# Optimization experiments

Measured on AMD Instinct MI355X. Metric: run time of the kernel, lower is better.

The kernel has to match this reference:

```python
import jax, jax.numpy as jnp
import numpy as np

B, E, H, O = 131072, 32, 32, 2

def setup_inputs() -> dict:
    key = jax.random.key(0)
    ks = jax.random.split(key, 12)
    f32 = jnp.float32
    inp = {
        "last_pos_rel": jax.random.normal(ks[0], (B, O), dtype=f32),
        "hidden_state": jax.random.normal(ks[1], (1, B, H), dtype=f32),
        "start_pos": jax.random.normal(ks[2], (B, O), dtype=f32),
        # spatial embedding Linear(2 -> 32)
        "W_se": jax.random.normal(ks[3], (E, O), dtype=f32) * 0.1,
        "b_se": jax.random.normal(ks[4], (E,), dtype=f32) * 0.1,
        # LSTM (input E -> hidden H), PyTorch layout: [4H, E] / [4H, H], gate order i,f,g,o
        "W_ih": jax.random.normal(ks[5], (4 * H, E), dtype=f32) * 0.1,
        "b_ih": jax.random.normal(ks[6], (4 * H,), dtype=f32) * 0.1,
        "W_hh": jax.random.normal(ks[7], (4 * H, H), dtype=f32) * 0.1,
        "b_hh": jax.random.normal(ks[8], (4 * H,), dtype=f32) * 0.1,
        # hidden2pos Linear(32 -> 2)
        "W_hp": jax.random.normal(ks[9], (O, H), dtype=f32) * 0.1,
        "b_hp": jax.random.normal(ks[10], (O,), dtype=f32) * 0.1,
        "seq_len": 60,
    }
    return inp


def reference(last_pos_rel, hidden_state, start_pos, W_se, b_se,
              W_ih, b_ih, W_hh, b_hh, W_hp, b_hp, seq_len):
    # dropout in eval mode -> identity
    h0 = hidden_state[0]                     # (B, H)  num_layers == 1
    c0 = jnp.zeros_like(h0)
    x0 = last_pos_rel @ W_se.T + b_se        # (B, E) spatial embedding
    b_gate = b_ih + b_hh                     # (4H,)

    def step(carry, _):
        h, c, x = carry
        gates = x @ W_ih.T + h @ W_hh.T + b_gate          # (B, 4H)
        i, f, g, o = jnp.split(gates, 4, axis=-1)         # PyTorch gate order
        c = jax.nn.sigmoid(f) * c + jax.nn.sigmoid(i) * jnp.tanh(g)
        h = jax.nn.sigmoid(o) * jnp.tanh(c)
        pos_rel = h @ W_hp.T + b_hp                        # (B, 2)
        x_next = pos_rel @ W_se.T + b_se                   # feed prediction back
        return (h, c, x_next), pos_rel

    (hT, cT, _), pred_traj_rel = jax.lax.scan(step, (h0, c0, x0), None, length=seq_len)
    # relative_to_abs: cumsum over time, add start_pos
    abs_traj = jnp.cumsum(pred_traj_rel, axis=0) + start_pos[None, :, :]  # (T, B, 2)
    return abs_traj, hT[None, :, :]
```

## Files before the change

kernel.cpp:

```cpp
#include <hip/hip_runtime.h>

typedef _Float16 half8  __attribute__((ext_vector_type(8)));
typedef __fp16   half2v __attribute__((ext_vector_type(2)));
typedef float    f32x4  __attribute__((ext_vector_type(4)));
typedef float    f32x2  __attribute__((ext_vector_type(2)));

#define L2E 1.44269504088896340736f
#define MFMA(a, b, c) __builtin_amdgcn_mfma_f32_16x16x32_f16((a), (b), (c), 0, 0, 0)

__global__ void precompute_kernel(const float* __restrict__ W_se,
                                  const float* __restrict__ b_se,
                                  const float* __restrict__ W_ih,
                                  const float* __restrict__ b_ih,
                                  const float* __restrict__ W_hh,
                                  const float* __restrict__ b_hh,
                                  const float* __restrict__ W_hp,
                                  const float* __restrict__ b_hp,
                                  float* __restrict__ ws) {
    int s = threadIdx.x;
    if (s >= 128) return;
    int gi = s >> 5, hf = (s >> 4) & 1, q = (s >> 2) & 3, r = s & 3;
    int o  = gi * 32 + 8 * q + 4 * hf + r;
    float w0 = 0.f, w1 = 0.f, bse = 0.f;
    for (int e = 0; e < 32; ++e) {
        float wi = W_ih[o * 32 + e];
        w0  += W_se[e * 2 + 0] * wi;
        w1  += W_se[e * 2 + 1] * wi;
        bse += b_se[e] * wi;
    }
    float sc = (gi == 2) ? 2.0f * L2E : -L2E;
    for (int k = 0; k < 32; ++k) {
        float whh = W_hh[o * 32 + k];
        ws[s * 32 + k]        = sc * (whh + W_hp[k] * w0 + W_hp[32 + k] * w1);
        ws[4096 + s * 32 + k] = sc * whh;
    }
    float bg = b_ih[o] + b_hh[o] + bse;
    ws[8192 + s] = sc * w0;
    ws[8320 + s] = sc * w1;
    ws[8448 + s] = sc * (bg + b_hp[0] * w0 + b_hp[1] * w1);
    ws[8576 + s] = sc * bg;
}

__device__ __forceinline__ void split8(const float* v, half8& hi, half8& lo) {
    #pragma unroll
    for (int p = 0; p < 4; ++p) {
        half2v hp = __builtin_amdgcn_cvt_pkrtz(v[2 * p], v[2 * p + 1]);
        hi[2 * p] = hp.x; hi[2 * p + 1] = hp.y;
        float l0 = v[2 * p]     - (float)hp.x;
        float l1 = v[2 * p + 1] - (float)hp.y;
        half2v lp2 = __builtin_amdgcn_cvt_pkrtz(l0, l1);
        lo[2 * p] = lp2.x; lo[2 * p + 1] = lp2.y;
    }
}

__device__ __forceinline__ void cvt8(const float* v, half8& hi) {
    #pragma unroll
    for (int p = 0; p < 4; ++p) {
        half2v hp = __builtin_amdgcn_cvt_pkrtz(v[2 * p], v[2 * p + 1]);
        hi[2 * p] = hp.x; hi[2 * p + 1] = hp.y;
    }
}

__global__ __launch_bounds__(256, 4) void lstm_kernel(
        const float* __restrict__ lp,
        const float* __restrict__ h0g,
        const float* __restrict__ sp,
        const float* __restrict__ Whp,
        const float* __restrict__ bhp,
        const float* __restrict__ ws,
        const int*   __restrict__ seqp,
        float* __restrict__ out, int Bn) {
    const int lane = threadIdx.x & 63;
    const int col  = lane & 15;
    const int q    = lane >> 4;
    const int tile = blockIdx.x * 4 + (threadIdx.x >> 6);
    const int base = tile * 16;
    if (base >= Bn) return;
    const int T = seqp[0];

    const float* Wcs  = ws;
    const float* Whhs = ws + 4096;
    const float* W00s = ws + 8192;
    const float* W01s = ws + 8320;
    const float* bg2q = ws + 8448 + 4 * q;
    const float* b0sq = ws + 8576 + 4 * q;

    half8 wh[8];
    #pragma unroll
    for (int t8 = 0; t8 < 8; ++t8) {
        float v[8];
        const float* p = Wcs + (size_t)(t8 * 16 + col) * 32 + 8 * q;
        #pragma unroll
        for (int i = 0; i < 8; ++i) v[i] = p[i];
        cvt8(v, wh[t8]);
    }
    half8 ph;
    {
        float v[8];
        #pragma unroll
        for (int i = 0; i < 8; ++i) v[i] = (col < 2) ? Whp[col * 32 + 8 * q + i] : 0.f;
        cvt8(v, ph);
    }
    const float pb0 = (q == 0) ? bhp[0] : 0.f;
    const float pb1 = (q == 0) ? bhp[1] : 0.f;

    half8 b0h, b0l;
    {
        float v[8];
        const float* p = h0g + (size_t)(base + col) * 32 + 8 * q;
        #pragma unroll
        for (int i = 0; i < 8; ++i) v[i] = p[i];
        split8(v, b0h, b0l);
    }
    half8 lph, lpl;
    #pragma unroll
    for (int i = 0; i < 8; ++i) { lph[i] = (_Float16)0.f; lpl[i] = (_Float16)0.f; }
    if (q == 0) {
        float l0 = lp[(size_t)(base + col) * 2 + 0];
        float l1 = lp[(size_t)(base + col) * 2 + 1];
        half2v x = __builtin_amdgcn_cvt_pkrtz(l0, l1);
        lph[0] = x.x; lph[1] = x.y;
        half2v y = __builtin_amdgcn_cvt_pkrtz(l0 - (float)x.x, l1 - (float)x.y);
        lpl[0] = y.x; lpl[1] = y.y;
    }

    f32x4 accg[8];
    #pragma unroll
    for (int t8 = 0; t8 < 8; ++t8) {
        f32x4 a = *(const f32x4*)(b0sq + t8 * 16);
        half8 ah;
        {
            float v[8];
            const float* p = Whhs + (size_t)(t8 * 16 + col) * 32 + 8 * q;
            #pragma unroll
            for (int i = 0; i < 8; ++i) v[i] = p[i];
            cvt8(v, ah);
        }
        a = MFMA(ah, b0h, a); a = MFMA(ah, b0l, a);
        half8 ch;
        #pragma unroll
        for (int i = 0; i < 8; ++i) ch[i] = (_Float16)0.f;
        if (q == 0) {
            half2v y = __builtin_amdgcn_cvt_pkrtz(W00s[t8 * 16 + col],
                                                  W01s[t8 * 16 + col]);
            ch[0] = y.x; ch[1] = y.y;
        }
        a = MFMA(ch, lph, a); a = MFMA(ch, lpl, a);
        accg[t8] = a;
    }

    f32x2 c2[4];
    #pragma unroll
    for (int i = 0; i < 4; ++i) c2[i] = (f32x2)0.f;
    float run0 = 0.f, run1 = 0.f;
    if (q == 0) {
        run0 = sp[(size_t)(base + col) * 2 + 0];
        run1 = sp[(size_t)(base + col) * 2 + 1];
    }

    float hn[8];
    #pragma unroll 1
    for (int n = 0; n < T; ++n) {
        #pragma unroll
        for (int hf = 0; hf < 2; ++hf) {
            #pragma unroll
            for (int rp = 0; rp < 2; ++rp) {
                const int idx = 2 * hf + rp;
                f32x2 gI, gF, gG, gO;
                gI.x = accg[0 + hf][2 * rp]; gI.y = accg[0 + hf][2 * rp + 1];
                gF.x = accg[2 + hf][2 * rp]; gF.y = accg[2 + hf][2 * rp + 1];
                gG.x = accg[4 + hf][2 * rp]; gG.y = accg[4 + hf][2 * rp + 1];
                gO.x = accg[6 + hf][2 * rp]; gO.y = accg[6 + hf][2 * rp + 1];
                f32x2 ei, ef, eg, eo;
                ei.x = __builtin_amdgcn_exp2f(gI.x); ei.y = __builtin_amdgcn_exp2f(gI.y);
                ef.x = __builtin_amdgcn_exp2f(gF.x); ef.y = __builtin_amdgcn_exp2f(gF.y);
                eg.x = __builtin_amdgcn_exp2f(gG.x); eg.y = __builtin_amdgcn_exp2f(gG.y);
                eo.x = __builtin_amdgcn_exp2f(gO.x); eo.y = __builtin_amdgcn_exp2f(gO.y);
                f32x2 Df = ef + 1.f;
                f32x2 P  = (ei + 1.f) * (eg + 1.f);
                f32x2 PD = P * Df;
                f32x2 R;
                R.x = __builtin_amdgcn_rcpf(PD.x); R.y = __builtin_amdgcn_rcpf(PD.y);
                f32x2 cn = ((eg - 1.f) * Df + c2[idx] * P) * R;
                c2[idx] = cn;
                f32x2 arg = cn * (2.f * L2E);
                f32x2 ec;
                ec.x = __builtin_amdgcn_exp2f(arg.x); ec.y = __builtin_amdgcn_exp2f(arg.y);
                f32x2 DDo = (ec + 1.f) * (eo + 1.f);
                f32x2 Rs;
                Rs.x = __builtin_amdgcn_rcpf(DDo.x); Rs.y = __builtin_amdgcn_rcpf(DDo.y);
                f32x2 h2 = (ec - 1.f) * Rs;
                hn[4 * hf + 2 * rp]     = h2.x;
                hn[4 * hf + 2 * rp + 1] = h2.y;
            }
        }
        half8 bh;
        cvt8(hn, bh);

        f32x4 ap;
        ap[0] = pb0; ap[1] = pb1; ap[2] = 0.f; ap[3] = 0.f;
        ap = MFMA(ph, bh, ap);

        #pragma unroll
        for (int t8 = 0; t8 < 8; ++t8) {
            f32x4 a = *(const f32x4*)(bg2q + t8 * 16);
            a = MFMA(wh[t8], bh, a);
            accg[t8] = a;
        }

        if (q == 0) {
            run0 += ap[0]; run1 += ap[1];
            float2 w2; w2.x = run0; w2.y = run1;
            *(float2*)(out + 2 * ((size_t)n * Bn + base + col)) = w2;
        }
    }

    {
        float* p = out + (size_t)T * Bn * 2 + (size_t)(base + col) * 32 + 8 * q;
        float4 v0, v1;
        v0.x = hn[0]; v0.y = hn[1]; v0.z = hn[2]; v0.w = hn[3];
        v1.x = hn[4]; v1.y = hn[5]; v1.z = hn[6]; v1.w = hn[7];
        *(float4*)(p)     = v0;
        *(float4*)(p + 4) = v1;
    }
}

extern "C" void kernel_launch(void* const* d_in, const int* in_sizes, int n_in,
                              void* d_out, int out_size, void* d_ws, size_t ws_size,
                              hipStream_t stream) {
    const float* last_pos_rel = (const float*)d_in[0];
    const float* hidden_state = (const float*)d_in[1];
    const float* start_pos    = (const float*)d_in[2];
    const float* W_se         = (const float*)d_in[3];
    const float* b_se         = (const float*)d_in[4];
    const float* W_ih         = (const float*)d_in[5];
    const float* b_ih         = (const float*)d_in[6];
    const float* W_hh         = (const float*)d_in[7];
    const float* b_hh         = (const float*)d_in[8];
    const float* W_hp         = (const float*)d_in[9];
    const float* b_hp         = (const float*)d_in[10];
    const int*   seq_len      = (const int*)d_in[11];

    float* out = (float*)d_out;
    float* ws  = (float*)d_ws;

    const int Bn = in_sizes[0] / 2;

    hipLaunchKernelGGL(precompute_kernel, dim3(1), dim3(128), 0, stream,
                       W_se, b_se, W_ih, b_ih, W_hh, b_hh, W_hp, b_hp, ws);

    const int ntiles = (Bn + 15) / 16;
    const int nblk   = (ntiles + 3) / 4;
    hipLaunchKernelGGL(lstm_kernel, dim3(nblk), dim3(256), 0, stream,
                       last_pos_rel, hidden_state, start_pos, W_hp, b_hp,
                       ws, seq_len, out, Bn);
}
```

Measured before the change: 212.1 us.

## Process two batch tiles per wavefront to interleave independent LSTM recurrences

Each wavefront now handles two 16-row batch tiles, A and B. It interleaves their gate activations and MFMA updates so the two independent dependency chains can hide each other's latency, and the register-held fp16 weight fragments serve both tiles. Launch bounds drop from 4 to 3 waves and the grid halves. The final hidden state is now written from the fp16-rounded values instead of the fp32 ones, which loses precision, and the kernel has no guard when baseB lies past the end of the batch.

```diff
diff --git a/kernel.cpp b/kernel.cpp
--- a/kernel.cpp
+++ b/kernel.cpp
@@ -53,15 +53,7 @@
     }
 }
 
-__device__ __forceinline__ void cvt8(const float* v, half8& hi) {
-    #pragma unroll
-    for (int p = 0; p < 4; ++p) {
-        half2v hp = __builtin_amdgcn_cvt_pkrtz(v[2 * p], v[2 * p + 1]);
-        hi[2 * p] = hp.x; hi[2 * p + 1] = hp.y;
-    }
-}
-
-__global__ __launch_bounds__(256, 4) void lstm_kernel(
+__global__ __launch_bounds__(256, 3) void lstm_kernel(
         const float* __restrict__ lp,
         const float* __restrict__ h0g,
         const float* __restrict__ sp,
@@ -70,12 +62,12 @@
         const float* __restrict__ ws,
         const int*   __restrict__ seqp,
         float* __restrict__ out, int Bn) {
-    const int lane = threadIdx.x & 63;
-    const int col  = lane & 15;
-    const int q    = lane >> 4;
-    const int tile = blockIdx.x * 4 + (threadIdx.x >> 6);
-    const int base = tile * 16;
-    if (base >= Bn) return;
+    const int lane  = threadIdx.x & 63;
+    const int col   = lane & 15;
+    const int q     = lane >> 4;
+    const int baseA = (blockIdx.x * 8 + (threadIdx.x >> 6) * 2) * 16;
+    const int baseB = baseA + 16;
+    if (baseA >= Bn) return;
     const int T = seqp[0];
 
     const float* Wcs  = ws;
@@ -88,140 +80,176 @@
     half8 wh[8];
     #pragma unroll
     for (int t8 = 0; t8 < 8; ++t8) {
-        float v[8];
         const float* p = Wcs + (size_t)(t8 * 16 + col) * 32 + 8 * q;
         #pragma unroll
-        for (int i = 0; i < 8; ++i) v[i] = p[i];
-        cvt8(v, wh[t8]);
+        for (int pp = 0; pp < 4; ++pp) {
+            half2v h2 = __builtin_amdgcn_cvt_pkrtz(p[2 * pp], p[2 * pp + 1]);
+            wh[t8][2 * pp] = h2.x; wh[t8][2 * pp + 1] = h2.y;
+        }
     }
     half8 ph;
-    {
-        float v[8];
-        #pragma unroll
-        for (int i = 0; i < 8; ++i) v[i] = (col < 2) ? Whp[col * 32 + 8 * q + i] : 0.f;
-        cvt8(v, ph);
+    #pragma unroll
+    for (int pp = 0; pp < 4; ++pp) {
+        float v0 = (col < 2) ? Whp[col * 32 + 8 * q + 2 * pp]     : 0.f;
+        float v1 = (col < 2) ? Whp[col * 32 + 8 * q + 2 * pp + 1] : 0.f;
+        half2v h2 = __builtin_amdgcn_cvt_pkrtz(v0, v1);
+        ph[2 * pp] = h2.x; ph[2 * pp + 1] = h2.y;
     }
     const float pb0 = (q == 0) ? bhp[0] : 0.f;
     const float pb1 = (q == 0) ? bhp[1] : 0.f;
 
-    half8 b0h, b0l;
+    f32x4 accgA[8], accgB[8];
     {
-        float v[8];
-        const float* p = h0g + (size_t)(base + col) * 32 + 8 * q;
-        #pragma unroll
-        for (int i = 0; i < 8; ++i) v[i] = p[i];
-        split8(v, b0h, b0l);
-    }
-    half8 lph, lpl;
-    #pragma unroll
-    for (int i = 0; i < 8; ++i) { lph[i] = (_Float16)0.f; lpl[i] = (_Float16)0.f; }
-    if (q == 0) {
-        float l0 = lp[(size_t)(base + col) * 2 + 0];
-        float l1 = lp[(size_t)(base + col) * 2 + 1];
-        half2v x = __builtin_amdgcn_cvt_pkrtz(l0, l1);
-        lph[0] = x.x; lph[1] = x.y;
-        half2v y = __builtin_amdgcn_cvt_pkrtz(l0 - (float)x.x, l1 - (float)x.y);
-        lpl[0] = y.x; lpl[1] = y.y;
-    }
-
-    f32x4 accg[8];
-    #pragma unroll
-    for (int t8 = 0; t8 < 8; ++t8) {
-        f32x4 a = *(const f32x4*)(b0sq + t8 * 16);
-        half8 ah;
+        half8 bhA0, blA0, bhB0, blB0;
         {
             float v[8];
-            const float* p = Whhs + (size_t)(t8 * 16 + col) * 32 + 8 * q;
-            #pragma unroll
-            for (int i = 0; i < 8; ++i) v[i] = p[i];
-            cvt8(v, ah);
-        }
-        a = MFMA(ah, b0h, a); a = MFMA(ah, b0l, a);
-        half8 ch;
-        #pragma unroll
-        for (int i = 0; i < 8; ++i) ch[i] = (_Float16)0.f;
+            const float* pa = h0g + (size_t)(baseA + col) * 32 + 8 * q;
+            #pragma unroll
+            for (int i = 0; i < 8; ++i) v[i] = pa[i];
+            split8(v, bhA0, blA0);
+            const float* pb = h0g + (size_t)(baseB + col) * 32 + 8 * q;
+            #pragma unroll
+            for (int i = 0; i < 8; ++i) v[i] = pb[i];
+            split8(v, bhB0, blB0);
+        }
+        half8 lphA, lplA, lphB, lplB;
+        #pragma unroll
+        for (int i = 0; i < 8; ++i) {
+            lphA[i] = (_Float16)0.f; lplA[i] = (_Float16)0.f;
+            lphB[i] = (_Float16)0.f; lplB[i] = (_Float16)0.f;
+        }
         if (q == 0) {
-            half2v y = __builtin_amdgcn_cvt_pkrtz(W00s[t8 * 16 + col],
-                                                  W01s[t8 * 16 + col]);
-            ch[0] = y.x; ch[1] = y.y;
-        }
-        a = MFMA(ch, lph, a); a = MFMA(ch, lpl, a);
-        accg[t8] = a;
-    }
-
-    f32x2 c2[4];
-    #pragma unroll
-    for (int i = 0; i < 4; ++i) c2[i] = (f32x2)0.f;
-    float run0 = 0.f, run1 = 0.f;
+            float a0 = lp[(size_t)(baseA + col) * 2 + 0];
+            float a1 = lp[(size_t)(baseA + col) * 2 + 1];
+            half2v x = __builtin_amdgcn_cvt_pkrtz(a0, a1);
+            lphA[0] = x.x; lphA[1] = x.y;
+            half2v y = __builtin_amdgcn_cvt_pkrtz(a0 - (float)x.x, a1 - (float)x.y);
+            lplA[0] = y.x; lplA[1] = y.y;
+            float b0v = lp[(size_t)(baseB + col) * 2 + 0];
+            float b1v = lp[(size_t)(baseB + col) * 2 + 1];
+            half2v xb = __builtin_amdgcn_cvt_pkrtz(b0v, b1v);
+            lphB[0] = xb.x; lphB[1] = xb.y;
+            half2v yb = __builtin_amdgcn_cvt_pkrtz(b0v - (float)xb.x, b1v - (float)xb.y);
+            lplB[0] = yb.x; lplB[1] = yb.y;
+        }
+        #pragma unroll
+        for (int t8 = 0; t8 < 8; ++t8) {
+            f32x4 bias0 = *(const f32x4*)(b0sq + t8 * 16);
+            half8 ah;
+            {
+                const float* p = Whhs + (size_t)(t8 * 16 + col) * 32 + 8 * q;
+                #pragma unroll
+                for (int pp = 0; pp < 4; ++pp) {
+                    half2v h2 = __builtin_amdgcn_cvt_pkrtz(p[2 * pp], p[2 * pp + 1]);
+                    ah[2 * pp] = h2.x; ah[2 * pp + 1] = h2.y;
+                }
+            }
+            half8 ch;
+            #pragma unroll
+            for (int i = 0; i < 8; ++i) ch[i] = (_Float16)0.f;
+            if (q == 0) {
+                half2v y = __builtin_amdgcn_cvt_pkrtz(W00s[t8 * 16 + col],
+                                                      W01s[t8 * 16 + col]);
+                ch[0] = y.x; ch[1] = y.y;
+            }
+            f32x4 aA = bias0, aB = bias0;
+            aA = MFMA(ah, bhA0, aA); aA = MFMA(ah, blA0, aA);
+            aA = MFMA(ch, lphA, aA); aA = MFMA(ch, lplA, aA);
+            aB = MFMA(ah, bhB0, aB); aB = MFMA(ah, blB0, aB);
+            aB = MFMA(ch, lphB, aB); aB = MFMA(ch, lplB, aB);
+            accgA[t8] = aA; accgB[t8] = aB;
+        }
+    }
+
+    f32x2 c2A[4], c2B[4];
+    #pragma unroll
+    for (int i = 0; i < 4; ++i) { c2A[i] = (f32x2)0.f; c2B[i] = (f32x2)0.f; }
+    float runA0 = 0.f, runA1 = 0.f, runB0 = 0.f, runB1 = 0.f;
     if (q == 0) {
-        run0 = sp[(size_t)(base + col) * 2 + 0];
-        run1 = sp[(size_t)(base + col) * 2 + 1];
-    }
-
-    float hn[8];
+        runA0 = sp[(size_t)(baseA + col) * 2 + 0];
+        runA1 = sp[(size_t)(baseA + col) * 2 + 1];
+        runB0 = sp[(size_t)(baseB + col) * 2 + 0];
+        runB1 = sp[(size_t)(baseB + col) * 2 + 1];
+    }
+
+    half8 bhA, bhB;
+
+    auto act2 = [&](f32x4* accg, f32x2* c2, half8& bh, int hf, int rp) {
+        const int idx = 2 * hf + rp;
+        f32x2 gI, gF, gG, gO;
+        gI.x = accg[0 + hf][2 * rp]; gI.y = accg[0 + hf][2 * rp + 1];
+        gF.x = accg[2 + hf][2 * rp]; gF.y = accg[2 + hf][2 * rp + 1];
+        gG.x = accg[4 + hf][2 * rp]; gG.y = accg[4 + hf][2 * rp + 1];
+        gO.x = accg[6 + hf][2 * rp]; gO.y = accg[6 + hf][2 * rp + 1];
+        f32x2 ei, ef, eg, eo;
+        ei.x = __builtin_amdgcn_exp2f(gI.x); ei.y = __builtin_amdgcn_exp2f(gI.y);
+        ef.x = __builtin_amdgcn_exp2f(gF.x); ef.y = __builtin_amdgcn_exp2f(gF.y);
+        eg.x = __builtin_amdgcn_exp2f(gG.x); eg.y = __builtin_amdgcn_exp2f(gG.y);
+        eo.x = __builtin_amdgcn_exp2f(gO.x); eo.y = __builtin_amdgcn_exp2f(gO.y);
+        f32x2 Df = ef + 1.f;
+        f32x2 P  = (ei + 1.f) * (eg + 1.f);
+        f32x2 PD = P * Df;
+        f32x2 R;
+        R.x = __builtin_amdgcn_rcpf(PD.x); R.y = __builtin_amdgcn_rcpf(PD.y);
+        f32x2 cn = ((eg - 1.f) * Df + c2[idx] * P) * R;
+        c2[idx] = cn;
+        f32x2 arg = cn * (2.f * L2E);
+        f32x2 ec;
+        ec.x = __builtin_amdgcn_exp2f(arg.x); ec.y = __builtin_amdgcn_exp2f(arg.y);
+        f32x2 DDo = (ec + 1.f) * (eo + 1.f);
+        f32x2 Rs;
+        Rs.x = __builtin_amdgcn_rcpf(DDo.x); Rs.y = __builtin_amdgcn_rcpf(DDo.y);
+        f32x2 h2 = (ec - 1.f) * Rs;
+        half2v hp = __builtin_amdgcn_cvt_pkrtz(h2.x, h2.y);
+        bh[2 * idx] = hp.x; bh[2 * idx + 1] = hp.y;
+    };
+
     #pragma unroll 1
     for (int n = 0; n < T; ++n) {
         #pragma unroll
         for (int hf = 0; hf < 2; ++hf) {
             #pragma unroll
             for (int rp = 0; rp < 2; ++rp) {
-                const int idx = 2 * hf + rp;
-                f32x2 gI, gF, gG, gO;
-                gI.x = accg[0 + hf][2 * rp]; gI.y = accg[0 + hf][2 * rp + 1];
-                gF.x = accg[2 + hf][2 * rp]; gF.y = accg[2 + hf][2 * rp + 1];
-                gG.x = accg[4 + hf][2 * rp]; gG.y = accg[4 + hf][2 * rp + 1];
-                gO.x = accg[6 + hf][2 * rp]; gO.y = accg[6 + hf][2 * rp + 1];
-                f32x2 ei, ef, eg, eo;
-                ei.x = __builtin_amdgcn_exp2f(gI.x); ei.y = __builtin_amdgcn_exp2f(gI.y);
-                ef.x = __builtin_amdgcn_exp2f(gF.x); ef.y = __builtin_amdgcn_exp2f(gF.y);
-                eg.x = __builtin_amdgcn_exp2f(gG.x); eg.y = __builtin_amdgcn_exp2f(gG.y);
-                eo.x = __builtin_amdgcn_exp2f(gO.x); eo.y = __builtin_amdgcn_exp2f(gO.y);
-                f32x2 Df = ef + 1.f;
-                f32x2 P  = (ei + 1.f) * (eg + 1.f);
-                f32x2 PD = P * Df;
-                f32x2 R;
-                R.x = __builtin_amdgcn_rcpf(PD.x); R.y = __builtin_amdgcn_rcpf(PD.y);
-                f32x2 cn = ((eg - 1.f) * Df + c2[idx] * P) * R;
-                c2[idx] = cn;
-                f32x2 arg = cn * (2.f * L2E);
-                f32x2 ec;
-                ec.x = __builtin_amdgcn_exp2f(arg.x); ec.y = __builtin_amdgcn_exp2f(arg.y);
-                f32x2 DDo = (ec + 1.f) * (eo + 1.f);
-                f32x2 Rs;
-                Rs.x = __builtin_amdgcn_rcpf(DDo.x); Rs.y = __builtin_amdgcn_rcpf(DDo.y);
-                f32x2 h2 = (ec - 1.f) * Rs;
-                hn[4 * hf + 2 * rp]     = h2.x;
-                hn[4 * hf + 2 * rp + 1] = h2.y;
+                act2(accgA, c2A, bhA, hf, rp);
+                act2(accgB, c2B, bhB, hf, rp);
             }
         }
-        half8 bh;
-        cvt8(hn, bh);
-
-        f32x4 ap;
-        ap[0] = pb0; ap[1] = pb1; ap[2] = 0.f; ap[3] = 0.f;
-        ap = MFMA(ph, bh, ap);
+
+        f32x4 apA, apB;
+        apA[0] = pb0; apA[1] = pb1; apA[2] = 0.f; apA[3] = 0.f;
+        apB = apA;
+        apA = MFMA(ph, bhA, apA);
+        apB = MFMA(ph, bhB, apB);
 
         #pragma unroll
         for (int t8 = 0; t8 < 8; ++t8) {
-            f32x4 a = *(const f32x4*)(bg2q + t8 * 16);
-            a = MFMA(wh[t8], bh, a);
-            accg[t8] = a;
+            f32x4 bt = *(const f32x4*)(bg2q + t8 * 16);
+            accgA[t8] = MFMA(wh[t8], bhA, bt);
+            accgB[t8] = MFMA(wh[t8], bhB, bt);
         }
 
         if (q == 0) {
-            run0 += ap[0]; run1 += ap[1];
-            float2 w2; w2.x = run0; w2.y = run1;
-            *(float2*)(out + 2 * ((size_t)n * Bn + base + col)) = w2;
+            runA0 += apA[0]; runA1 += apA[1];
+            runB0 += apB[0]; runB1 += apB[1];
+            float2 wA; wA.x = runA0; wA.y = runA1;
+            float2 wB; wB.x = runB0; wB.y = runB1;
+            *(float2*)(out + 2 * ((size_t)n * Bn + baseA + col)) = wA;
+            *(float2*)(out + 2 * ((size_t)n * Bn + baseB + col)) = wB;
         }
     }
 
     {
-        float* p = out + (size_t)T * Bn * 2 + (size_t)(base + col) * 32 + 8 * q;
+        float* pa = out + (size_t)T * Bn * 2 + (size_t)(baseA + col) * 32 + 8 * q;
+        float* pb = out + (size_t)T * Bn * 2 + (size_t)(baseB + col) * 32 + 8 * q;
         float4 v0, v1;
-        v0.x = hn[0]; v0.y = hn[1]; v0.z = hn[2]; v0.w = hn[3];
-        v1.x = hn[4]; v1.y = hn[5]; v1.z = hn[6]; v1.w = hn[7];
-        *(float4*)(p)     = v0;
-        *(float4*)(p + 4) = v1;
+        v0.x = (float)bhA[0]; v0.y = (float)bhA[1]; v0.z = (float)bhA[2]; v0.w = (float)bhA[3];
+        v1.x = (float)bhA[4]; v1.y = (float)bhA[5]; v1.z = (float)bhA[6]; v1.w = (float)bhA[7];
+        *(float4*)(pa)     = v0;
+        *(float4*)(pa + 4) = v1;
+        v0.x = (float)bhB[0]; v0.y = (float)bhB[1]; v0.z = (float)bhB[2]; v0.w = (float)bhB[3];
+        v1.x = (float)bhB[4]; v1.y = (float)bhB[5]; v1.z = (float)bhB[6]; v1.w = (float)bhB[7];
+        *(float4*)(pb)     = v0;
+        *(float4*)(pb + 4) = v1;
     }
 }
 
@@ -250,7 +278,7 @@
                        W_se, b_se, W_ih, b_ih, W_hh, b_hh, W_hp, b_hp, ws);
 
     const int ntiles = (Bn + 15) / 16;
-    const int nblk   = (ntiles + 3) / 4;
+    const int nblk   = (ntiles + 7) / 8;
     hipLaunchKernelGGL(lstm_kernel, dim3(nblk), dim3(256), 0, stream,
                        last_pos_rel, hidden_state, start_pos, W_hp, b_hp,
                        ws, seq_len, out, Bn);
```

New measurement: 216.2 us. About the same (+1.9%).
